# Kernel tuning notes

Measured on AMD Instinct MI355X. Metric: run time of the kernel, lower is better.

## Reference

```python
import jax, jax.numpy as jnp
import numpy as np

B = 131072      # batch
NC = 1000       # num_classes
A = 128         # action_dim
ELD = 128       # embedding_latent_dim
VQN = 512       # vq_num_embeddings
VQD = 64        # vq_embedding_dim
SQUISH = 1.0
CC = 0.25       # commitment cost

def _he(k, fi, fo):
    lim = float(np.sqrt(6.0 / fi))
    return jax.random.uniform(k, (fi, fo), jnp.float32, -lim, lim)

def setup_inputs() -> dict:
    key = jax.random.key(0)
    ks = jax.random.split(key, 16)
    cb_lim = float(np.sqrt(3.0 / VQD))  # variance_scaling fan_in uniform
    return {
        "obs": jax.random.randint(ks[0], (B,), 0, NC),
        "embed": jax.random.normal(ks[1], (NC, ELD), jnp.float32) * 0.02,
        "W1": _he(ks[2], ELD, 128), "b1": jnp.zeros((128,), jnp.float32),
        "W2": _he(ks[3], 128, 128), "b2": jnp.zeros((128,), jnp.float32),
        "W3": _he(ks[4], 128, 128), "b3": jnp.zeros((128,), jnp.float32),
        "Wp": _he(ks[5], 128, VQD), "bp": jnp.zeros((VQD,), jnp.float32),
        "codebook": jax.random.uniform(ks[6], (VQN, VQD), jnp.float32, -cb_lim, cb_lim),
        "Wa": jax.random.normal(ks[7], (VQD, A), jnp.float32) * 0.01, "ba": jnp.zeros((A,), jnp.float32),
        "Ws": jax.random.normal(ks[8], (VQD, A), jnp.float32) * 0.01, "bs": jnp.zeros((A,), jnp.float32),
        "Wc1": _he(ks[9], VQD, 128), "bc1": jnp.zeros((128,), jnp.float32),
        "Wc2": _he(ks[10], 128, 128), "bc2": jnp.zeros((128,), jnp.float32),
        "Wc3": _he(ks[11], 128, 32), "bc3": jnp.zeros((32,), jnp.float32),
        "Wc4": _he(ks[12], 32, 1), "bc4": jnp.zeros((1,), jnp.float32),
    }

def reference(obs, embed, W1, b1, W2, b2, W3, b3, Wp, bp, codebook,
              Wa, ba, Ws, bs, Wc1, bc1, Wc2, bc2, Wc3, bc3, Wc4, bc4):
    # embedding lookup + small dense stack
    y = jnp.take(embed, obs, axis=0)                 # [B, 128]
    z = jax.nn.relu(y @ W1 + b1)
    z = jax.nn.relu(z @ W2 + b2)
    z = jax.nn.relu(z @ W3 + b3)
    z = z @ Wp + bp                                  # [B, 64] project to vq dim
    # VQ: pairwise squared distances, argmin, gather (== one_hot @ codebook)
    d = (jnp.sum(z * z, axis=1, keepdims=True)
         - 2.0 * (z @ codebook.T)
         + jnp.sum(codebook * codebook, axis=1))     # [B, 512]
    idx = jnp.argmin(d, axis=1)                      # [B]
    quant = jnp.take(codebook, idx, axis=0)          # [B, 64]
    q = z + jax.lax.stop_gradient(quant - z)         # straight-through
    e_loss = jnp.mean((jax.lax.stop_gradient(q) - z) ** 2)
    q_loss = jnp.mean((q - jax.lax.stop_gradient(z)) ** 2)
    vq_loss = q_loss + CC * e_loss
    # actor heads (pi = MvNormalDiag(actor_mean, scale_diag); return params)
    actor_mean = jax.nn.sigmoid(q @ Wa + ba)
    scale_diag = jax.nn.sigmoid(q @ Ws + bs) * SQUISH + 1e-8
    # critic head
    c = jax.nn.sigmoid(q @ Wc1 + bc1)
    c = jax.nn.sigmoid(c @ Wc2 + bc2)
    c = jax.nn.sigmoid(c @ Wc3 + bc3)
    critic = jnp.squeeze(c @ Wc4 + bc4, axis=-1)     # [B]
    return actor_mean, scale_diag, critic, vq_loss, idx
```

## Files before the change

kernel.cpp:

```cpp
#include <hip/hip_runtime.h>
#include <math.h>


typedef float f4 __attribute__((ext_vector_type(4)));
typedef float f2 __attribute__((ext_vector_type(2)));

__device__ __forceinline__ float sigmoidf_(float x){ return 1.0f/(1.0f + expf(-x)); }

__global__ __launch_bounds__(256, 4) void compute_kernel(
    const float* __restrict__ embed,
    const float* __restrict__ W1, const float* __restrict__ b1,
    const float* __restrict__ W2, const float* __restrict__ b2,
    const float* __restrict__ W3, const float* __restrict__ b3,
    const float* __restrict__ Wp, const float* __restrict__ bp,
    const float* __restrict__ cb,
    const float* __restrict__ Wa, const float* __restrict__ ba,
    const float* __restrict__ Ws, const float* __restrict__ bs,
    const float* __restrict__ Wc1, const float* __restrict__ bc1,
    const float* __restrict__ Wc2, const float* __restrict__ bc2,
    const float* __restrict__ Wc3, const float* __restrict__ bc3,
    const float* __restrict__ Wc4, const float* __restrict__ bc4,
    float* __restrict__ am_c, float* __restrict__ sd_c,
    float* __restrict__ cr_c, int* __restrict__ idx_t, float* __restrict__ e_t,
    float* __restrict__ loss_slot, int VQN, int NC, int nTB)
{
    const int bid = blockIdx.x;
    const int t   = threadIdx.x;
    if (bid == 0 && t == 0) *loss_slot = 0.0f;

    __shared__ double U[2][128], V[2][128];
    __shared__ double part[2][8][128];
    __shared__ double zp2[2][64];
    __shared__ float  qv2[2][64];
    __shared__ double rda[2][4];
    __shared__ int    ria[2][4];
    __shared__ int    widx2[2];
    __shared__ float  qvh[2][64];
    __shared__ float  fpart[2][4][128];
    __shared__ float  gpart[2][2][128];
    __shared__ float  h1s[2][128], h2s[2][128], h3s[2][32];

    if (bid < nTB) {
        const int c0  = bid * 2;
        const int c1  = (c0 + 1 < NC) ? c0 + 1 : NC - 1;
        const int cls = t >> 7;
        const int r   = t & 127;
        const int q4  = (t & 31) << 2;
        const int h   = t >> 5;

        if (t < 128) U[0][t] = (double)embed[(size_t)c0 * 128 + t];
        else         U[1][r] = (double)embed[(size_t)c1 * 128 + r];
        __syncthreads();

#define TRUNK2(Wm, bv, IN, OUT)                                               \
        {                                                                     \
            double aA0 = (h == 0) ? (double)bv[q4+0] : 0.0;                   \
            double aA1 = (h == 0) ? (double)bv[q4+1] : 0.0;                   \
            double aA2 = (h == 0) ? (double)bv[q4+2] : 0.0;                   \
            double aA3 = (h == 0) ? (double)bv[q4+3] : 0.0;                   \
            double aB0 = aA0, aB1 = aA1, aB2 = aA2, aB3 = aA3;                \
            _Pragma("unroll")                                                 \
            for (int s = 0; s < 16; ++s) {                                    \
                int i = h + (s << 3);                                         \
                f4 w = *(const f4*)(Wm + (size_t)i * 128 + q4);               \
                double w0 = (double)w.x, w1 = (double)w.y;                    \
                double w2 = (double)w.z, w3 = (double)w.w;                    \
                double xA = IN[0][i], xB = IN[1][i];                          \
                aA0 = fma(xA, w0, aA0);  aB0 = fma(xB, w0, aB0);              \
                aA1 = fma(xA, w1, aA1);  aB1 = fma(xB, w1, aB1);              \
                aA2 = fma(xA, w2, aA2);  aB2 = fma(xB, w2, aB2);              \
                aA3 = fma(xA, w3, aA3);  aB3 = fma(xB, w3, aB3);              \
            }                                                                 \
            part[0][h][q4+0] = aA0; part[0][h][q4+1] = aA1;                   \
            part[0][h][q4+2] = aA2; part[0][h][q4+3] = aA3;                   \
            part[1][h][q4+0] = aB0; part[1][h][q4+1] = aB1;                   \
            part[1][h][q4+2] = aB2; part[1][h][q4+3] = aB3;                   \
        }                                                                     \
        __syncthreads();                                                      \
        {                                                                     \
            double acc = ((part[cls][0][r] + part[cls][1][r])                 \
                        + (part[cls][2][r] + part[cls][3][r]))                \
                       + ((part[cls][4][r] + part[cls][5][r])                 \
                        + (part[cls][6][r] + part[cls][7][r]));               \
            OUT[cls][r] = acc > 0.0 ? acc : 0.0;                              \
        }                                                                     \
        __syncthreads();

        TRUNK2(W1, b1, U, V)
        TRUNK2(W2, b2, V, U)
        TRUNK2(W3, b3, U, V)
#undef TRUNK2

        {
            const int q4p = (r & 15) << 2;
            const int hp  = r >> 4;
            double a0 = (hp == 0) ? (double)bp[q4p+0] : 0.0;
            double a1 = (hp == 0) ? (double)bp[q4p+1] : 0.0;
            double a2 = (hp == 0) ? (double)bp[q4p+2] : 0.0;
            double a3 = (hp == 0) ? (double)bp[q4p+3] : 0.0;
            #pragma unroll
            for (int s = 0; s < 16; ++s) {
                int i = hp + (s << 3);
                f4 w = *(const f4*)(Wp + (size_t)i * 64 + q4p);
                double x = V[cls][i];
                a0 = fma(x, (double)w.x, a0);
                a1 = fma(x, (double)w.y, a1);
                a2 = fma(x, (double)w.z, a2);
                a3 = fma(x, (double)w.w, a3);
            }
            part[cls][hp][q4p+0] = a0; part[cls][hp][q4p+1] = a1;
            part[cls][hp][q4p+2] = a2; part[cls][hp][q4p+3] = a3;
        }
        __syncthreads();
        if (r < 64) {
            zp2[cls][r] = ((part[cls][0][r] + part[cls][1][r])
                         + (part[cls][2][r] + part[cls][3][r]))
                        + ((part[cls][4][r] + part[cls][5][r])
                         + (part[cls][6][r] + part[cls][7][r]));
        }
        __syncthreads();

        double bestA = 1e300, bestB = 1e300; int biA = 0, biB = 0;
        for (int k = t; k < VQN; k += 256) {
            const float* crow = cb + (size_t)k * 64;
            double sA0 = 0.0, sA1 = 0.0, sB0 = 0.0, sB1 = 0.0;
            #pragma unroll
            for (int j4 = 0; j4 < 16; ++j4) {
                f4 v = *(const f4*)(crow + (j4 << 2));
                int j = j4 << 2;
                double w0 = (double)v.x, w1 = (double)v.y;
                double w2 = (double)v.z, w3 = (double)v.w;
                double dA0 = zp2[0][j+0] - w0, dA1 = zp2[0][j+1] - w1;
                double dA2 = zp2[0][j+2] - w2, dA3 = zp2[0][j+3] - w3;
                double dB0 = zp2[1][j+0] - w0, dB1 = zp2[1][j+1] - w1;
                double dB2 = zp2[1][j+2] - w2, dB3 = zp2[1][j+3] - w3;
                sA0 = fma(dA0, dA0, sA0);  sA1 = fma(dA1, dA1, sA1);
                sA0 = fma(dA2, dA2, sA0);  sA1 = fma(dA3, dA3, sA1);
                sB0 = fma(dB0, dB0, sB0);  sB1 = fma(dB1, dB1, sB1);
                sB0 = fma(dB2, dB2, sB0);  sB1 = fma(dB3, dB3, sB1);
            }
            double sA = sA0 + sA1, sB = sB0 + sB1;
            if (sA < bestA) { bestA = sA; biA = k; }
            if (sB < bestB) { bestB = sB; biB = k; }
        }
        for (int off = 32; off > 0; off >>= 1) {
            double od = __shfl_down(bestA, off);
            int    oi = __shfl_down(biA, off);
            if (od < bestA || (od == bestA && oi < biA)) { bestA = od; biA = oi; }
            od = __shfl_down(bestB, off);
            oi = __shfl_down(biB, off);
            if (od < bestB || (od == bestB && oi < biB)) { bestB = od; biB = oi; }
        }
        {
            int wv = t >> 6;
            if ((t & 63) == 0) {
                rda[0][wv] = bestA; ria[0][wv] = biA;
                rda[1][wv] = bestB; ria[1][wv] = biB;
            }
        }
        __syncthreads();
        if (t < 2) {
            double b0 = rda[t][0]; int i0 = ria[t][0];
            for (int wv = 1; wv < 4; ++wv) {
                if (rda[t][wv] < b0 || (rda[t][wv] == b0 && ria[t][wv] < i0)) {
                    b0 = rda[t][wv]; i0 = ria[t][wv];
                }
            }
            widx2[t] = i0;
        }
        __syncthreads();
        const int widxA = widx2[0], widxB = widx2[1];
        if (t < 64)       qv2[0][t]      = cb[(size_t)widxA * 64 + t];
        else if (t < 128) qv2[1][t - 64] = cb[(size_t)widxB * 64 + (t - 64)];
        __syncthreads();

        if (t == 0) {
            idx_t[c0] = widxA;
            double e0 = 0.0, e1 = 0.0;
            for (int j = 0; j < 64; j += 2) {
                double d0 = (double)qv2[0][j]   - zp2[0][j];
                double d1 = (double)qv2[0][j+1] - zp2[0][j+1];
                e0 = fma(d0, d0, e0); e1 = fma(d1, d1, e1);
            }
            e_t[c0] = (float)(e0 + e1);
        }
        if (t == 128 && c1 != c0) {
            idx_t[c1] = widxB;
            double e0 = 0.0, e1 = 0.0;
            for (int j = 0; j < 64; j += 2) {
                double d0 = (double)qv2[1][j]   - zp2[1][j];
                double d1 = (double)qv2[1][j+1] - zp2[1][j+1];
                e0 = fma(d0, d0, e0); e1 = fma(d1, d1, e1);
            }
            e_t[c1] = (float)(e0 + e1);
        }
    } else {
        const int g  = t >> 7;
        const int tt = t & 127;
        int k = (bid - nTB) * 2 + g;
        const int kk = (k < VQN) ? k : VQN - 1;
        const int q4 = (tt & 31) << 2;

        if (tt < 64) qvh[g][tt] = cb[(size_t)kk * 64 + tt];
        __syncthreads();

        {
            const int m  = tt >> 6;
            const int hh = (tt >> 5) & 1;
            const float* Wm = m ? Ws : Wa;
            const float* bm = m ? bs : ba;
            float a0 = hh ? 0.0f : bm[q4+0];
            float a1 = hh ? 0.0f : bm[q4+1];
            float a2 = hh ? 0.0f : bm[q4+2];
            float a3 = hh ? 0.0f : bm[q4+3];
            #pragma unroll
            for (int s = 0; s < 32; ++s) {
                f4 w = *(const f4*)(Wm + (size_t)(hh + (s << 1)) * 128 + q4);
                float qj = qvh[g][hh + (s << 1)];
                a0 = fmaf(qj, w.x, a0);
                a1 = fmaf(qj, w.y, a1);
                a2 = fmaf(qj, w.z, a2);
                a3 = fmaf(qj, w.w, a3);
            }
            fpart[g][tt >> 5][q4+0] = a0; fpart[g][tt >> 5][q4+1] = a1;
            fpart[g][tt >> 5][q4+2] = a2; fpart[g][tt >> 5][q4+3] = a3;
        }
        __syncthreads();

        if (tt < 64) {
            const int hh = tt >> 5;
            float a0 = hh ? 0.0f : bc1[q4+0];
            float a1 = hh ? 0.0f : bc1[q4+1];
            float a2 = hh ? 0.0f : bc1[q4+2];
            float a3 = hh ? 0.0f : bc1[q4+3];
            #pragma unroll
            for (int s = 0; s < 32; ++s) {
                f4 w = *(const f4*)(Wc1 + (size_t)(hh + (s << 1)) * 128 + q4);
                float qj = qvh[g][hh + (s << 1)];
                a0 = fmaf(qj, w.x, a0);
                a1 = fmaf(qj, w.y, a1);
                a2 = fmaf(qj, w.z, a2);
                a3 = fmaf(qj, w.w, a3);
            }
            gpart[g][hh][q4+0] = a0; gpart[g][hh][q4+1] = a1;
            gpart[g][hh][q4+2] = a2; gpart[g][hh][q4+3] = a3;
        } else {
            int o = (tt - 64) << 1;
            am_c[(size_t)kk * 128 + o]     = sigmoidf_(fpart[g][0][o]   + fpart[g][1][o]);
            am_c[(size_t)kk * 128 + o + 1] = sigmoidf_(fpart[g][0][o+1] + fpart[g][1][o+1]);
            sd_c[(size_t)kk * 128 + o]     = sigmoidf_(fpart[g][2][o]   + fpart[g][3][o])   * 1.0f + 1e-8f;
            sd_c[(size_t)kk * 128 + o + 1] = sigmoidf_(fpart[g][2][o+1] + fpart[g][3][o+1]) * 1.0f + 1e-8f;
        }
        __syncthreads();
        h1s[g][tt] = sigmoidf_(gpart[g][0][tt] + gpart[g][1][tt]);
        __syncthreads();

        {
            const int o2 = (tt & 63) << 1;
            const int hh = tt >> 6;
            float a0 = hh ? 0.0f : bc2[o2+0];
            float a1 = hh ? 0.0f : bc2[o2+1];
            #pragma unroll
            for (int s = 0; s < 64; ++s) {
                f2 w = *(const f2*)(Wc2 + (size_t)(hh + (s << 1)) * 128 + o2);
                float x = h1s[g][hh + (s << 1)];
                a0 = fmaf(x, w.x, a0);
                a1 = fmaf(x, w.y, a1);
            }
            gpart[g][hh][o2+0] = a0; gpart[g][hh][o2+1] = a1;
        }
        __syncthreads();
        h2s[g][tt] = sigmoidf_(gpart[g][0][tt] + gpart[g][1][tt]);
        __syncthreads();

        if (tt < 32) {
            const int o2 = (tt & 15) << 1;
            const int hh = tt >> 4;
            float a0 = hh ? 0.0f : bc3[o2+0];
            float a1 = hh ? 0.0f : bc3[o2+1];
            #pragma unroll
            for (int s = 0; s < 64; ++s) {
                f2 w = *(const f2*)(Wc3 + (size_t)(hh + (s << 1)) * 32 + o2);
                float x = h2s[g][hh + (s << 1)];
                a0 = fmaf(x, w.x, a0);
                a1 = fmaf(x, w.y, a1);
            }
            gpart[g][hh][o2+0] = a0; gpart[g][hh][o2+1] = a1;
        }
        __syncthreads();
        if (tt < 32) h3s[g][tt] = sigmoidf_(gpart[g][0][tt] + gpart[g][1][tt]);
        __syncthreads();

        if (tt == 0) {
            float l4 = bc4[0];
            for (int i = 0; i < 32; ++i) l4 = fmaf(h3s[g][i], Wc4[i], l4);
            cr_c[kk] = l4;
        }
    }
}

__global__ __launch_bounds__(256) void scatter_kernel(
    const int* __restrict__ obs,
    const f4* __restrict__ am_c, const f4* __restrict__ sd_c,
    const float* __restrict__ cr_c, const int* __restrict__ idx_t,
    const float* __restrict__ e_t,
    f4* __restrict__ out_vec, float* __restrict__ out_critic,
    float* __restrict__ out_idx, float* __restrict__ out_loss,
    int B, float scale)
{
    __shared__ float red[256];
    const int vecBlocks = (B * 32) / 256;
    if ((int)blockIdx.x < vecBlocks) {
        int gid = blockIdx.x * 256 + threadIdx.x;
        int b = gid >> 5;
        int j = gid & 31;
        int k = idx_t[obs[b]];
        size_t row = (size_t)k * 32 + j;
        __builtin_nontemporal_store(am_c[row], &out_vec[gid]);
        __builtin_nontemporal_store(sd_c[row], &out_vec[(size_t)B * 32 + gid]);
        return;
    }
    int b = (blockIdx.x - vecBlocks) * 256 + threadIdx.x;
    float e = 0.0f;
    if (b < B) {
        int o = obs[b];
        int k = idx_t[o];
        __builtin_nontemporal_store(cr_c[k], &out_critic[b]);
        __builtin_nontemporal_store((float)k, &out_idx[b]);
        e = e_t[o];
    }
    red[threadIdx.x] = e;
    __syncthreads();
    for (int s = 128; s > 0; s >>= 1) {
        if (threadIdx.x < s) red[threadIdx.x] += red[threadIdx.x + s];
        __syncthreads();
    }
    if (threadIdx.x == 0) atomicAdd(out_loss, red[0] * scale);
}

extern "C" void kernel_launch(void* const* d_in, const int* in_sizes, int n_in,
                              void* d_out, int out_size, void* d_ws, size_t ws_size,
                              hipStream_t stream)
{
    const int*   obs   = (const int*)  d_in[0];
    const float* embed = (const float*)d_in[1];
    const float* W1    = (const float*)d_in[2];
    const float* b1    = (const float*)d_in[3];
    const float* W2    = (const float*)d_in[4];
    const float* b2    = (const float*)d_in[5];
    const float* W3    = (const float*)d_in[6];
    const float* b3    = (const float*)d_in[7];
    const float* Wp    = (const float*)d_in[8];
    const float* bp    = (const float*)d_in[9];
    const float* cb    = (const float*)d_in[10];
    const float* Wa    = (const float*)d_in[11];
    const float* ba    = (const float*)d_in[12];
    const float* Ws    = (const float*)d_in[13];
    const float* bs    = (const float*)d_in[14];
    const float* Wc1   = (const float*)d_in[15];
    const float* bc1   = (const float*)d_in[16];
    const float* Wc2   = (const float*)d_in[17];
    const float* bc2   = (const float*)d_in[18];
    const float* Wc3   = (const float*)d_in[19];
    const float* bc3   = (const float*)d_in[20];
    const float* Wc4   = (const float*)d_in[21];
    const float* bc4   = (const float*)d_in[22];

    const int B   = in_sizes[0];
    const int NC  = in_sizes[1] / 128;
    const int VQN = in_sizes[10] / 64;

    float* am_c = (float*)d_ws;
    float* sd_c = am_c + (size_t)VQN * 128;
    float* cr_c = sd_c + (size_t)VQN * 128;
    float* e_t  = cr_c + VQN;
    int*   idx_t = (int*)(e_t + NC);

    float* out = (float*)d_out;
    const size_t cr_off   = (size_t)B * 256;
    const size_t loss_off = cr_off + (size_t)B;
    const size_t idx_off  = loss_off + 1;

    const int nTB = (NC + 1) / 2;
    const int nHB = (VQN + 1) / 2;

    compute_kernel<<<nTB + nHB, 256, 0, stream>>>(
        embed, W1, b1, W2, b2, W3, b3, Wp, bp, cb,
        Wa, ba, Ws, bs, Wc1, bc1, Wc2, bc2, Wc3, bc3, Wc4, bc4,
        am_c, sd_c, cr_c, idx_t, e_t, out + loss_off, VQN, NC, nTB);

    const int vecBlocks    = (B * 32) / 256;
    const int scalarBlocks = (B + 255) / 256;
    scatter_kernel<<<vecBlocks + scalarBlocks, 256, 0, stream>>>(
        obs, (const f4*)am_c, (const f4*)sd_c, cr_c, idx_t, e_t,
        (f4*)out, out + cr_off, out + idx_off, out + loss_off,
        B, 1.25f / ((float)B * 64.0f));
}
```

Before: 264.1 us.

## Process eight classes per block with one warp-of-32 per class in trunk

The trunk blocks now handle eight classes each, with a 32-lane group owning one class and computing every MLP output column itself instead of splitting the K dimension across eight groups and reducing through shared memory. This removes the partial-sum shared buffers and most barriers, and the codebook argmin becomes a 32-lane shuffle reduction. In exchange each thread does a longer serial double-precision loop over the inputs, the trunk launches fewer blocks, and the occupancy hint in the launch bounds is dropped.

```diff
diff --git a/kernel.cpp b/kernel.cpp
--- a/kernel.cpp
+++ b/kernel.cpp
@@ -7,7 +7,7 @@
 
 __device__ __forceinline__ float sigmoidf_(float x){ return 1.0f/(1.0f + expf(-x)); }
 
-__global__ __launch_bounds__(256, 4) void compute_kernel(
+__global__ __launch_bounds__(256) void compute_kernel(
     const float* __restrict__ embed,
     const float* __restrict__ W1, const float* __restrict__ b1,
     const float* __restrict__ W2, const float* __restrict__ b2,
@@ -28,171 +28,138 @@
     const int t   = threadIdx.x;
     if (bid == 0 && t == 0) *loss_slot = 0.0f;
 
-    __shared__ double U[2][128], V[2][128];
-    __shared__ double part[2][8][128];
-    __shared__ double zp2[2][64];
-    __shared__ float  qv2[2][64];
-    __shared__ double rda[2][4];
-    __shared__ int    ria[2][4];
-    __shared__ int    widx2[2];
+    __shared__ double X[8][128], Y[8][128];
+    __shared__ double zp8[8][64];
+    __shared__ float  qv8[8][64];
     __shared__ float  qvh[2][64];
     __shared__ float  fpart[2][4][128];
     __shared__ float  gpart[2][2][128];
     __shared__ float  h1s[2][128], h2s[2][128], h3s[2][32];
 
     if (bid < nTB) {
-        const int c0  = bid * 2;
-        const int c1  = (c0 + 1 < NC) ? c0 + 1 : NC - 1;
-        const int cls = t >> 7;
-        const int r   = t & 127;
-        const int q4  = (t & 31) << 2;
-        const int h   = t >> 5;
-
-        if (t < 128) U[0][t] = (double)embed[(size_t)c0 * 128 + t];
-        else         U[1][r] = (double)embed[(size_t)c1 * 128 + r];
-        __syncthreads();
-
-#define TRUNK2(Wm, bv, IN, OUT)                                               \
+        const int g  = t >> 5;
+        const int q  = t & 31;
+        int c = bid * 8 + g;
+        if (c >= NC) c = NC - 1;
+        const int o4 = q << 2;
+
+        {
+            f4 e = *(const f4*)(embed + (size_t)c * 128 + o4);
+            X[g][o4+0] = (double)e.x; X[g][o4+1] = (double)e.y;
+            X[g][o4+2] = (double)e.z; X[g][o4+3] = (double)e.w;
+        }
+        __syncthreads();
+
+#define LAYER(Wm, bv, IN, OUT)                                                \
         {                                                                     \
-            double aA0 = (h == 0) ? (double)bv[q4+0] : 0.0;                   \
-            double aA1 = (h == 0) ? (double)bv[q4+1] : 0.0;                   \
-            double aA2 = (h == 0) ? (double)bv[q4+2] : 0.0;                   \
-            double aA3 = (h == 0) ? (double)bv[q4+3] : 0.0;                   \
-            double aB0 = aA0, aB1 = aA1, aB2 = aA2, aB3 = aA3;                \
+            f4 bb = *(const f4*)(bv + o4);                                    \
+            double a0[4] = {(double)bb.x,(double)bb.y,(double)bb.z,(double)bb.w};\
+            double a1[4] = {0.0,0.0,0.0,0.0};                                 \
+            double a2[4] = {0.0,0.0,0.0,0.0};                                 \
+            double a3[4] = {0.0,0.0,0.0,0.0};                                 \
+            _Pragma("unroll 8")                                               \
+            for (int s = 0; s < 32; ++s) {                                    \
+                int i = s << 2;                                               \
+                f4 w0 = *(const f4*)(Wm + (size_t)(i+0) * 128 + o4);          \
+                f4 w1 = *(const f4*)(Wm + (size_t)(i+1) * 128 + o4);          \
+                f4 w2 = *(const f4*)(Wm + (size_t)(i+2) * 128 + o4);          \
+                f4 w3 = *(const f4*)(Wm + (size_t)(i+3) * 128 + o4);          \
+                double x0 = IN[g][i+0], x1 = IN[g][i+1];                      \
+                double x2 = IN[g][i+2], x3 = IN[g][i+3];                      \
+                a0[0]=fma(x0,(double)w0.x,a0[0]); a0[1]=fma(x0,(double)w0.y,a0[1]);\
+                a0[2]=fma(x0,(double)w0.z,a0[2]); a0[3]=fma(x0,(double)w0.w,a0[3]);\
+                a1[0]=fma(x1,(double)w1.x,a1[0]); a1[1]=fma(x1,(double)w1.y,a1[1]);\
+                a1[2]=fma(x1,(double)w1.z,a1[2]); a1[3]=fma(x1,(double)w1.w,a1[3]);\
+                a2[0]=fma(x2,(double)w2.x,a2[0]); a2[1]=fma(x2,(double)w2.y,a2[1]);\
+                a2[2]=fma(x2,(double)w2.z,a2[2]); a2[3]=fma(x2,(double)w2.w,a2[3]);\
+                a3[0]=fma(x3,(double)w3.x,a3[0]); a3[1]=fma(x3,(double)w3.y,a3[1]);\
+                a3[2]=fma(x3,(double)w3.z,a3[2]); a3[3]=fma(x3,(double)w3.w,a3[3]);\
+            }                                                                 \
             _Pragma("unroll")                                                 \
-            for (int s = 0; s < 16; ++s) {                                    \
-                int i = h + (s << 3);                                         \
-                f4 w = *(const f4*)(Wm + (size_t)i * 128 + q4);               \
-                double w0 = (double)w.x, w1 = (double)w.y;                    \
-                double w2 = (double)w.z, w3 = (double)w.w;                    \
-                double xA = IN[0][i], xB = IN[1][i];                          \
-                aA0 = fma(xA, w0, aA0);  aB0 = fma(xB, w0, aB0);              \
-                aA1 = fma(xA, w1, aA1);  aB1 = fma(xB, w1, aB1);              \
-                aA2 = fma(xA, w2, aA2);  aB2 = fma(xB, w2, aB2);              \
-                aA3 = fma(xA, w3, aA3);  aB3 = fma(xB, w3, aB3);              \
+            for (int o = 0; o < 4; ++o) {                                     \
+                double acc = (a0[o] + a1[o]) + (a2[o] + a3[o]);               \
+                OUT[g][o4 + o] = acc > 0.0 ? acc : 0.0;                       \
             }                                                                 \
-            part[0][h][q4+0] = aA0; part[0][h][q4+1] = aA1;                   \
-            part[0][h][q4+2] = aA2; part[0][h][q4+3] = aA3;                   \
-            part[1][h][q4+0] = aB0; part[1][h][q4+1] = aB1;                   \
-            part[1][h][q4+2] = aB2; part[1][h][q4+3] = aB3;                   \
         }                                                                     \
-        __syncthreads();                                                      \
-        {                                                                     \
-            double acc = ((part[cls][0][r] + part[cls][1][r])                 \
-                        + (part[cls][2][r] + part[cls][3][r]))                \
-                       + ((part[cls][4][r] + part[cls][5][r])                 \
-                        + (part[cls][6][r] + part[cls][7][r]));               \
-            OUT[cls][r] = acc > 0.0 ? acc : 0.0;                              \
-        }                                                                     \
-        __syncthreads();
-
-        TRUNK2(W1, b1, U, V)
-        TRUNK2(W2, b2, V, U)
-        TRUNK2(W3, b3, U, V)
-#undef TRUNK2
-
-        {
-            const int q4p = (r & 15) << 2;
-            const int hp  = r >> 4;
-            double a0 = (hp == 0) ? (double)bp[q4p+0] : 0.0;
-            double a1 = (hp == 0) ? (double)bp[q4p+1] : 0.0;
-            double a2 = (hp == 0) ? (double)bp[q4p+2] : 0.0;
-            double a3 = (hp == 0) ? (double)bp[q4p+3] : 0.0;
-            #pragma unroll
-            for (int s = 0; s < 16; ++s) {
-                int i = hp + (s << 3);
-                f4 w = *(const f4*)(Wp + (size_t)i * 64 + q4p);
-                double x = V[cls][i];
-                a0 = fma(x, (double)w.x, a0);
-                a1 = fma(x, (double)w.y, a1);
-                a2 = fma(x, (double)w.z, a2);
-                a3 = fma(x, (double)w.w, a3);
-            }
-            part[cls][hp][q4p+0] = a0; part[cls][hp][q4p+1] = a1;
-            part[cls][hp][q4p+2] = a2; part[cls][hp][q4p+3] = a3;
-        }
-        __syncthreads();
-        if (r < 64) {
-            zp2[cls][r] = ((part[cls][0][r] + part[cls][1][r])
-                         + (part[cls][2][r] + part[cls][3][r]))
-                        + ((part[cls][4][r] + part[cls][5][r])
-                         + (part[cls][6][r] + part[cls][7][r]));
-        }
-        __syncthreads();
-
-        double bestA = 1e300, bestB = 1e300; int biA = 0, biB = 0;
-        for (int k = t; k < VQN; k += 256) {
+        __syncthreads();
+
+        LAYER(W1, b1, X, Y)
+        LAYER(W2, b2, Y, X)
+        LAYER(W3, b3, X, Y)
+#undef LAYER
+
+        if (q < 16) {
+            const int o4p = q << 2;
+            f4 bb = *(const f4*)(bp + o4p);
+            double a0[4] = {(double)bb.x,(double)bb.y,(double)bb.z,(double)bb.w};
+            double a1[4] = {0.0,0.0,0.0,0.0};
+            double a2[4] = {0.0,0.0,0.0,0.0};
+            double a3[4] = {0.0,0.0,0.0,0.0};
+            #pragma unroll 8
+            for (int s = 0; s < 32; ++s) {
+                int i = s << 2;
+                f4 w0 = *(const f4*)(Wp + (size_t)(i+0) * 64 + o4p);
+                f4 w1 = *(const f4*)(Wp + (size_t)(i+1) * 64 + o4p);
+                f4 w2 = *(const f4*)(Wp + (size_t)(i+2) * 64 + o4p);
+                f4 w3 = *(const f4*)(Wp + (size_t)(i+3) * 64 + o4p);
+                double x0 = Y[g][i+0], x1 = Y[g][i+1];
+                double x2 = Y[g][i+2], x3 = Y[g][i+3];
+                a0[0]=fma(x0,(double)w0.x,a0[0]); a0[1]=fma(x0,(double)w0.y,a0[1]);
+                a0[2]=fma(x0,(double)w0.z,a0[2]); a0[3]=fma(x0,(double)w0.w,a0[3]);
+                a1[0]=fma(x1,(double)w1.x,a1[0]); a1[1]=fma(x1,(double)w1.y,a1[1]);
+                a1[2]=fma(x1,(double)w1.z,a1[2]); a1[3]=fma(x1,(double)w1.w,a1[3]);
+                a2[0]=fma(x2,(double)w2.x,a2[0]); a2[1]=fma(x2,(double)w2.y,a2[1]);
+                a2[2]=fma(x2,(double)w2.z,a2[2]); a2[3]=fma(x2,(double)w2.w,a2[3]);
+                a3[0]=fma(x3,(double)w3.x,a3[0]); a3[1]=fma(x3,(double)w3.y,a3[1]);
+                a3[2]=fma(x3,(double)w3.z,a3[2]); a3[3]=fma(x3,(double)w3.w,a3[3]);
+            }
+            #pragma unroll
+            for (int o = 0; o < 4; ++o)
+                zp8[g][o4p + o] = (a0[o] + a1[o]) + (a2[o] + a3[o]);
+        }
+        __syncthreads();
+
+        double best = 1e300; int bi = 0;
+        for (int k = q; k < VQN; k += 32) {
             const float* crow = cb + (size_t)k * 64;
-            double sA0 = 0.0, sA1 = 0.0, sB0 = 0.0, sB1 = 0.0;
+            double s0 = 0.0, s1 = 0.0;
             #pragma unroll
             for (int j4 = 0; j4 < 16; ++j4) {
                 f4 v = *(const f4*)(crow + (j4 << 2));
                 int j = j4 << 2;
-                double w0 = (double)v.x, w1 = (double)v.y;
-                double w2 = (double)v.z, w3 = (double)v.w;
-                double dA0 = zp2[0][j+0] - w0, dA1 = zp2[0][j+1] - w1;
-                double dA2 = zp2[0][j+2] - w2, dA3 = zp2[0][j+3] - w3;
-                double dB0 = zp2[1][j+0] - w0, dB1 = zp2[1][j+1] - w1;
-                double dB2 = zp2[1][j+2] - w2, dB3 = zp2[1][j+3] - w3;
-                sA0 = fma(dA0, dA0, sA0);  sA1 = fma(dA1, dA1, sA1);
-                sA0 = fma(dA2, dA2, sA0);  sA1 = fma(dA3, dA3, sA1);
-                sB0 = fma(dB0, dB0, sB0);  sB1 = fma(dB1, dB1, sB1);
-                sB0 = fma(dB2, dB2, sB0);  sB1 = fma(dB3, dB3, sB1);
-            }
-            double sA = sA0 + sA1, sB = sB0 + sB1;
-            if (sA < bestA) { bestA = sA; biA = k; }
-            if (sB < bestB) { bestB = sB; biB = k; }
-        }
-        for (int off = 32; off > 0; off >>= 1) {
-            double od = __shfl_down(bestA, off);
-            int    oi = __shfl_down(biA, off);
-            if (od < bestA || (od == bestA && oi < biA)) { bestA = od; biA = oi; }
-            od = __shfl_down(bestB, off);
-            oi = __shfl_down(biB, off);
-            if (od < bestB || (od == bestB && oi < biB)) { bestB = od; biB = oi; }
-        }
-        {
-            int wv = t >> 6;
-            if ((t & 63) == 0) {
-                rda[0][wv] = bestA; ria[0][wv] = biA;
-                rda[1][wv] = bestB; ria[1][wv] = biB;
-            }
-        }
-        __syncthreads();
-        if (t < 2) {
-            double b0 = rda[t][0]; int i0 = ria[t][0];
-            for (int wv = 1; wv < 4; ++wv) {
-                if (rda[t][wv] < b0 || (rda[t][wv] == b0 && ria[t][wv] < i0)) {
-                    b0 = rda[t][wv]; i0 = ria[t][wv];
-                }
-            }
-            widx2[t] = i0;
-        }
-        __syncthreads();
-        const int widxA = widx2[0], widxB = widx2[1];
-        if (t < 64)       qv2[0][t]      = cb[(size_t)widxA * 64 + t];
-        else if (t < 128) qv2[1][t - 64] = cb[(size_t)widxB * 64 + (t - 64)];
-        __syncthreads();
-
-        if (t == 0) {
-            idx_t[c0] = widxA;
+                double d0 = zp8[g][j+0] - (double)v.x;
+                double d1 = zp8[g][j+1] - (double)v.y;
+                double d2 = zp8[g][j+2] - (double)v.z;
+                double d3 = zp8[g][j+3] - (double)v.w;
+                s0 = fma(d0, d0, s0);  s1 = fma(d1, d1, s1);
+                s0 = fma(d2, d2, s0);  s1 = fma(d3, d3, s1);
+            }
+            double s = s0 + s1;
+            if (s < best) { best = s; bi = k; }
+        }
+        for (int off = 16; off > 0; off >>= 1) {
+            double od = __shfl_down(best, off, 32);
+            int    oi = __shfl_down(bi, off, 32);
+            if (od < best || (od == best && oi < bi)) { best = od; bi = oi; }
+        }
+        const int widx = __shfl(bi, 0, 32);
+
+        if (q < 16) {
+            f4 cq = *(const f4*)(cb + (size_t)widx * 64 + (q << 2));
+            qv8[g][(q<<2)+0] = cq.x; qv8[g][(q<<2)+1] = cq.y;
+            qv8[g][(q<<2)+2] = cq.z; qv8[g][(q<<2)+3] = cq.w;
+        }
+        __syncthreads();
+
+        if (q == 0) {
+            idx_t[c] = widx;
             double e0 = 0.0, e1 = 0.0;
             for (int j = 0; j < 64; j += 2) {
-                double d0 = (double)qv2[0][j]   - zp2[0][j];
-                double d1 = (double)qv2[0][j+1] - zp2[0][j+1];
+                double d0 = (double)qv8[g][j]   - zp8[g][j];
+                double d1 = (double)qv8[g][j+1] - zp8[g][j+1];
                 e0 = fma(d0, d0, e0); e1 = fma(d1, d1, e1);
             }
-            e_t[c0] = (float)(e0 + e1);
-        }
-        if (t == 128 && c1 != c0) {
-            idx_t[c1] = widxB;
-            double e0 = 0.0, e1 = 0.0;
-            for (int j = 0; j < 64; j += 2) {
-                double d0 = (double)qv2[1][j]   - zp2[1][j];
-                double d1 = (double)qv2[1][j+1] - zp2[1][j+1];
-                e0 = fma(d0, d0, e0); e1 = fma(d1, d1, e1);
-            }
-            e_t[c1] = (float)(e0 + e1);
+            e_t[c] = (float)(e0 + e1);
         }
     } else {
         const int g  = t >> 7;
@@ -381,7 +348,7 @@
     const size_t loss_off = cr_off + (size_t)B;
     const size_t idx_off  = loss_off + 1;
 
-    const int nTB = (NC + 1) / 2;
+    const int nTB = (NC + 7) / 8;
     const int nHB = (VQN + 1) / 2;
 
     compute_kernel<<<nTB + nHB, 256, 0, stream>>>(
```

Result: slower. 294.7 us (+11.6%).
